# Kernel tuning notes

Measured on AMD Instinct MI355X. Metric: run time of the kernel, lower is better.

## Reference

```python
import jax, jax.numpy as jnp
import numpy as np

EMBED_DIM = 512
N_HEADS = 8
D_K = EMBED_DIM // N_HEADS

def _xavier(key, shape):
    fan_in, fan_out = shape[1], shape[0]
    limit = np.sqrt(6.0 / (fan_in + fan_out))
    return jax.random.uniform(key, shape, jnp.float32, -limit, limit)

def setup_inputs() -> dict:
    key = jax.random.key(0)
    ks = jax.random.split(key, 8)
    B, S, D = 2, 4096, EMBED_DIM
    return {
        "q": jax.random.normal(ks[0], (B, S, D), jnp.float32),
        "k": jax.random.normal(ks[1], (B, S, D), jnp.float32),
        "v": jax.random.normal(ks[2], (B, S, D), jnp.float32),
        "W_q": _xavier(ks[3], (D, D)),
        "W_k": _xavier(ks[4], (D, D)),
        "W_v": _xavier(ks[5], (D, D)),
        "W_o": _xavier(ks[6], (D, D)),
        "b_o": jnp.zeros((D,), jnp.float32),
    }

def reference(q, k, v, W_q, W_k, W_v, W_o, b_o):
    B, Sq, D = q.shape
    Sk = k.shape[1]
    # linear projections (torch Linear: x @ W.T)
    qh = (q @ W_q.T).reshape(B, Sq, N_HEADS, D_K).transpose(0, 2, 1, 3)
    kh = (k @ W_k.T).reshape(B, Sk, N_HEADS, D_K).transpose(0, 2, 1, 3)
    vh = (v @ W_v.T).reshape(B, Sk, N_HEADS, D_K).transpose(0, 2, 1, 3)
    scores = jnp.einsum('bhqd,bhkd->bhqk', qh, kh)  # [B,H,Sq,Sk]
    causal = jnp.triu(jnp.ones((Sq, Sk), bool), k=1)
    scores = jnp.where(causal, -jnp.inf, scores)
    attn = jax.nn.softmax(scores / np.sqrt(D_K), axis=-1)
    ctx = jnp.einsum('bhqk,bhkd->bhqd', attn, vh)
    ctx = ctx.transpose(0, 2, 1, 3).reshape(B, Sq, D)
    return ctx @ W_o.T + b_o
```

## Files before the change

### kernel.cpp

```cpp
#include <hip/hip_runtime.h>

typedef _Float16 f16;
typedef _Float16 f16x8 __attribute__((ext_vector_type(8)));
typedef _Float16 f16x4 __attribute__((ext_vector_type(4)));
typedef _Float16 f16x2 __attribute__((ext_vector_type(2)));
typedef float f32x4 __attribute__((ext_vector_type(4)));
typedef float f32x16 __attribute__((ext_vector_type(16)));
typedef unsigned int u32x2 __attribute__((ext_vector_type(2)));

#define S_TOK 4096
#define NB 2
#define NH 8
#define DKH 64
#define DMODEL 512

static __device__ __forceinline__ f32x4 mfma16(f16x8 a, f16x8 b, f32x4 c) {
    return __builtin_amdgcn_mfma_f32_16x16x32_f16(a, b, c, 0, 0, 0);
}
static __device__ __forceinline__ f32x16 mfma32(f16x8 a, f16x8 b, f32x16 c) {
    return __builtin_amdgcn_mfma_f32_32x32x16_f16(a, b, c, 0, 0, 0);
}
static __device__ __forceinline__ void gl16(const f16* g, f16* l) {
    __builtin_amdgcn_global_load_lds(
        (const __attribute__((address_space(1))) unsigned int*)g,
        (__attribute__((address_space(3))) unsigned int*)l, 16, 0, 0);
}

__global__ __launch_bounds__(256)
void proj_fused_kernel(const float* __restrict__ qx, const float* __restrict__ kx,
                       const float* __restrict__ vx,
                       const float* __restrict__ Wqp, const float* __restrict__ Wkp,
                       const float* __restrict__ Wvp,
                       f16* __restrict__ qo, f16* __restrict__ ko, f16* __restrict__ vo)
{
    const int mode = blockIdx.z;
    const float* x = (mode == 0) ? qx : (mode == 1) ? kx : vx;
    const float* W = (mode == 0) ? Wqp : (mode == 1) ? Wkp : Wvp;
    f16* out = (mode == 0) ? qo : (mode == 1) ? ko : vo;

    __shared__ f16 As[128 * 40];
    __shared__ f16 Bs[128 * 40];
    const int m0 = blockIdx.x * 128;
    const int n0 = blockIdx.y * 128;
    const int tid = threadIdx.x;
    const int wv = tid >> 6;
    const int lane = tid & 63;
    const int lr = lane & 15, lg = lane >> 4;
    const int wm = (wv >> 1) * 64, wn = (wv & 1) * 64;

    f32x4 acc[4][4];
#pragma unroll
    for (int i = 0; i < 4; ++i)
#pragma unroll
        for (int j = 0; j < 4; ++j) acc[i][j] = f32x4{0.f, 0.f, 0.f, 0.f};

    for (int kb = 0; kb < DMODEL; kb += 32) {
#pragma unroll
        for (int c = 0; c < 2; ++c) {
            const int chunk = tid + c * 256;
            const int row = chunk >> 2;
            const int col = (chunk & 3) * 8;
            const float* ga = x + (size_t)(m0 + row) * DMODEL + kb + col;
            float4 a0 = *(const float4*)ga;
            float4 a1 = *(const float4*)(ga + 4);
            f16x8 ha = { (f16)a0.x, (f16)a0.y, (f16)a0.z, (f16)a0.w,
                         (f16)a1.x, (f16)a1.y, (f16)a1.z, (f16)a1.w };
            *(f16x8*)(As + row * 40 + col) = ha;
            const float* gb = W + (size_t)(n0 + row) * DMODEL + kb + col;
            float4 b0 = *(const float4*)gb;
            float4 b1 = *(const float4*)(gb + 4);
            f16x8 hb = { (f16)b0.x, (f16)b0.y, (f16)b0.z, (f16)b0.w,
                         (f16)b1.x, (f16)b1.y, (f16)b1.z, (f16)b1.w };
            *(f16x8*)(Bs + row * 40 + col) = hb;
        }
        __syncthreads();
        f16x8 af[4], bf[4];
#pragma unroll
        for (int i = 0; i < 4; ++i)
            af[i] = *(const f16x8*)(As + (wm + 16 * i + lr) * 40 + 8 * lg);
#pragma unroll
        for (int j = 0; j < 4; ++j)
            bf[j] = *(const f16x8*)(Bs + (wn + 16 * j + lr) * 40 + 8 * lg);
#pragma unroll
        for (int i = 0; i < 4; ++i)
#pragma unroll
            for (int j = 0; j < 4; ++j)
                acc[i][j] = mfma16(af[i], bf[j], acc[i][j]);
        __syncthreads();
    }

#pragma unroll
    for (int i = 0; i < 4; ++i) {
        const int mbase = m0 + wm + 16 * i + 4 * lg;
#pragma unroll
        for (int j = 0; j < 4; ++j) {
            const int n = n0 + wn + 16 * j + lr;
            const int h = n >> 6, dk = n & 63;
            if (mode == 2) {
                const int b = mbase >> 12;
                const int s = mbase & 4095;
                f16x4 v4;
#pragma unroll
                for (int r = 0; r < 4; ++r) v4[r] = (f16)acc[i][j][r];
                *(f16x4*)(out + ((size_t)(b * NH + h) * DKH + dk) * S_TOK + s) = v4;
            } else {
                const float sc = (mode == 0) ? 0.1803368801111244f : 1.0f;
#pragma unroll
                for (int r = 0; r < 4; ++r) {
                    const int m = mbase + r;
                    const int b = m >> 12, s = m & 4095;
                    out[((size_t)(b * NH + h) * S_TOK + s) * DKH + dk] = (f16)(acc[i][j][r] * sc);
                }
            }
        }
    }
}

__global__ __launch_bounds__(256, 4)
void attn_kernel(const f16* __restrict__ qh, const f16* __restrict__ kh,
                 const f16* __restrict__ vt, f16* __restrict__ pO, float* __restrict__ pL)
{
    __shared__ f16 Ks[2][64 * 64];
    __shared__ f16 Vs[2][64 * 64];

    const int bid = blockIdx.x;
    const int bh = 2 * (bid & 7) + ((bid >> 3) & 1);
    const int j = (bid >> 4) & 31;
    const int cb = (bid >> 9) & 1;
    const int tid = threadIdx.x, wv = tid >> 6, lane = tid & 63;
    const int l31 = lane & 31, h = lane >> 5;
    const int swzl = (l31 & 7) ^ (((l31 >> 3) & 3) << 1);

    const f16* Qp = qh + (size_t)bh * S_TOK * DKH;
    const f16* Kp = kh + (size_t)bh * S_TOK * DKH;
    const f16* Vp = vt + (size_t)bh * DKH * S_TOK;

    const int srow = tid >> 3;
    const int sg = tid & 7;
    const int sgx = sg ^ ((srow & 7) ^ (((srow >> 3) & 3) << 1));

    int cur = 0;
    for (int seg = 0; seg < 2; ++seg) {
        const int qt = seg ? (31 - j) : j;
        const int cc = seg ? (3 - cb) : cb;
        const int T = 2 * qt + 2;
        const int tb = (cc * T) >> 2;
        const int te = ((cc + 1) * T) >> 2;
        const int qw = qt * 128 + 32 * wv + l31;
        const int unit = (bh * 32 + qt) * 4 + cc;

        f16x8 aq[4];
#pragma unroll
        for (int s = 0; s < 4; ++s)
            aq[s] = *(const f16x8*)(Qp + (size_t)qw * DKH + 16 * s + 8 * h);

        f32x16 accO0 = {}, accO1 = {};
        float mrow = -1e20f, lrow = 0.f;

        if (te > tb) {
            {
                const f16* kp1 = Kp + (size_t)(64 * tb + srow) * DKH + sgx * 8;
                gl16(kp1, &Ks[cur][wv * 512]);
                gl16(kp1 + 32 * DKH, &Ks[cur][2048 + wv * 512]);
                const f16* vp1 = Vp + (size_t)srow * S_TOK + 64 * tb + sgx * 8;
                gl16(vp1, &Vs[cur][wv * 512]);
                gl16(vp1 + (size_t)32 * S_TOK, &Vs[cur][2048 + wv * 512]);
            }
            for (int t = tb; t < te; ++t) {
                __syncthreads();
                if (t + 1 < te) {
                    const f16* kp1 = Kp + (size_t)(64 * (t + 1) + srow) * DKH + sgx * 8;
                    gl16(kp1, &Ks[cur ^ 1][wv * 512]);
                    gl16(kp1 + 32 * DKH, &Ks[cur ^ 1][2048 + wv * 512]);
                    const f16* vp1 = Vp + (size_t)srow * S_TOK + 64 * (t + 1) + sgx * 8;
                    gl16(vp1, &Vs[cur ^ 1][wv * 512]);
                    gl16(vp1 + (size_t)32 * S_TOK, &Vs[cur ^ 1][2048 + wv * 512]);
                }
                const f16* Kb = &Ks[cur][0];
                const f16* Vb = &Vs[cur][0];
                const bool diag = (t >= 2 * qt);

#pragma unroll
                for (int half = 0; half < 2; ++half) {
                    f32x16 accS = {};
                    __builtin_amdgcn_s_setprio(1);
#pragma unroll
                    for (int s = 0; s < 4; ++s) {
                        f16x8 ak = *(const f16x8*)(Kb + (32 * half + l31) * 64 +
                                                   ((2 * s + h) ^ swzl) * 8);
                        accS = mfma32(ak, aq[s], accS);
                    }
                    __builtin_amdgcn_s_setprio(0);

                    if (diag) {
#pragma unroll
                        for (int e = 0; e < 16; ++e) {
                            const int kvb = 64 * t + 32 * half + (e & 3) + 8 * (e >> 2) + 4 * h;
                            accS[e] = (kvb > qw) ? -1e30f : accS[e];
                        }
                    }

                    float m8a = fmaxf(fmaxf(accS[0], accS[1]), fmaxf(accS[2], accS[3]));
                    float m8b = fmaxf(fmaxf(accS[4], accS[5]), fmaxf(accS[6], accS[7]));
                    float m8c = fmaxf(fmaxf(accS[8], accS[9]), fmaxf(accS[10], accS[11]));
                    float m8d = fmaxf(fmaxf(accS[12], accS[13]), fmaxf(accS[14], accS[15]));
                    float tm = fmaxf(fmaxf(m8a, m8b), fmaxf(m8c, m8d));
                    tm = fmaxf(tm, __shfl_xor(tm, 32));
                    if (!__all(tm <= mrow + 8.f)) {
                        const float mn = fmaxf(mrow, tm);
                        const float sf = exp2f(mrow - mn);
                        lrow *= sf;
                        accO0 *= sf;  accO1 *= sf;
                        mrow = mn;
                    }

                    unsigned int Xd0[4], Xd1[4];
                    float ts4[4];
#pragma unroll
                    for (int g = 0; g < 4; ++g) {
                        float p0 = exp2f(accS[4 * g + 0] - mrow);
                        float p1 = exp2f(accS[4 * g + 1] - mrow);
                        float p2 = exp2f(accS[4 * g + 2] - mrow);
                        float p3 = exp2f(accS[4 * g + 3] - mrow);
                        ts4[g] = (p0 + p1) + (p2 + p3);
                        union { f16x2 hh; unsigned int u; } a0, a1;
                        a0.hh = f16x2{(f16)p0, (f16)p1};
                        a1.hh = f16x2{(f16)p2, (f16)p3};
                        Xd0[g] = a0.u;  Xd1[g] = a1.u;
                    }
                    float ts = (ts4[0] + ts4[1]) + (ts4[2] + ts4[3]);
                    ts += __shfl_xor(ts, 32);
                    lrow += ts;

                    __builtin_amdgcn_s_setprio(1);
#pragma unroll
                    for (int sp = 0; sp < 2; ++sp) {
                        const int spp = 2 * half + sp;
                        u32x2 rA = __builtin_amdgcn_permlane32_swap(Xd0[2 * sp], Xd0[2 * sp + 1], false, false);
                        u32x2 rB = __builtin_amdgcn_permlane32_swap(Xd1[2 * sp], Xd1[2 * sp + 1], false, false);
                        union { unsigned int u[4]; f16x8 v; } F;
                        F.u[0] = rA[0]; F.u[1] = rB[0]; F.u[2] = rA[1]; F.u[3] = rB[1];
                        f16x8 av0 = *(const f16x8*)(Vb + l31 * 64 + ((2 * spp + h) ^ swzl) * 8);
                        f16x8 av1 = *(const f16x8*)(Vb + (32 + l31) * 64 + ((2 * spp + h) ^ swzl) * 8);
                        accO0 = mfma32(av0, F.v, accO0);
                        accO1 = mfma32(av1, F.v, accO1);
                    }
                    __builtin_amdgcn_s_setprio(0);
                }
                cur ^= 1;
            }
        }

        const float invl = (lrow > 0.f) ? (1.f / lrow) : 0.f;
        f16* Ob = pO + ((size_t)unit * 128 + (32 * wv + l31)) * DKH;
#pragma unroll
        for (int g = 0; g < 4; ++g) {
            f16x4 o0, o1;
#pragma unroll
            for (int r = 0; r < 4; ++r) {
                o0[r] = (f16)(accO0[4 * g + r] * invl);
                o1[r] = (f16)(accO1[4 * g + r] * invl);
            }
            *(f16x4*)(Ob + 8 * g + 4 * h) = o0;
            *(f16x4*)(Ob + 32 + 8 * g + 4 * h) = o1;
        }
        if (h == 0)
            pL[unit * 128 + 32 * wv + l31] =
                (lrow > 0.f) ? (mrow + __log2f(lrow)) : -1e30f;
    }
}

__global__ __launch_bounds__(256)
void merge_kernel(const f16* __restrict__ pO, const float* __restrict__ pL,
                  f16* __restrict__ ctx)
{
    const int tid = threadIdx.x;
    const int R = blockIdx.x * 32 + (tid >> 3);
    const int dkg = tid & 7;
    const int bh = R >> 12, q = R & 4095;
    const int qt = q >> 7, qi = q & 127;
    const int ub = (bh * 32 + qt) * 4;

    float L[4];
#pragma unroll
    for (int c = 0; c < 4; ++c) L[c] = pL[(ub + c) * 128 + qi];
    float Lm = fmaxf(fmaxf(L[0], L[1]), fmaxf(L[2], L[3]));
    float w[4], wsum = 0.f;
#pragma unroll
    for (int c = 0; c < 4; ++c) { w[c] = exp2f(L[c] - Lm); wsum += w[c]; }
    const float inv = 1.f / wsum;

    float o[8];
#pragma unroll
    for (int i = 0; i < 8; ++i) o[i] = 0.f;
#pragma unroll
    for (int c = 0; c < 4; ++c) {
        f16x8 a = *(const f16x8*)(pO + ((size_t)(ub + c) * 128 + qi) * DKH + dkg * 8);
#pragma unroll
        for (int i = 0; i < 8; ++i) o[i] += w[c] * (float)a[i];
    }
    f16x8 ov;
#pragma unroll
    for (int i = 0; i < 8; ++i) ov[i] = (f16)(o[i] * inv);

    const int bb = bh >> 3, hh = bh & 7;
    *(f16x8*)(ctx + ((size_t)(bb * S_TOK + q)) * DMODEL + hh * DKH + dkg * 8) = ov;
}

__global__ __launch_bounds__(256)
void oproj_kernel(const f16* __restrict__ A, const float* __restrict__ W,
                  const float* __restrict__ bias, float* __restrict__ out)
{
    __shared__ f16 As[128 * 40];
    __shared__ f16 Bs[128 * 40];
    const int m0 = blockIdx.x * 128;
    const int n0 = blockIdx.y * 128;
    const int tid = threadIdx.x;
    const int wv = tid >> 6;
    const int lane = tid & 63;
    const int lr = lane & 15, lg = lane >> 4;
    const int wm = (wv >> 1) * 64, wn = (wv & 1) * 64;

    f32x4 acc[4][4];
#pragma unroll
    for (int i = 0; i < 4; ++i)
#pragma unroll
        for (int j = 0; j < 4; ++j) acc[i][j] = f32x4{0.f, 0.f, 0.f, 0.f};

    for (int kb = 0; kb < DMODEL; kb += 32) {
#pragma unroll
        for (int c = 0; c < 2; ++c) {
            const int chunk = tid + c * 256;
            const int row = chunk >> 2;
            const int col = (chunk & 3) * 8;
            *(f16x8*)(As + row * 40 + col) =
                *(const f16x8*)(A + (size_t)(m0 + row) * DMODEL + kb + col);
            const float* gb = W + (size_t)(n0 + row) * DMODEL + kb + col;
            float4 b0 = *(const float4*)gb;
            float4 b1 = *(const float4*)(gb + 4);
            f16x8 hb = { (f16)b0.x, (f16)b0.y, (f16)b0.z, (f16)b0.w,
                         (f16)b1.x, (f16)b1.y, (f16)b1.z, (f16)b1.w };
            *(f16x8*)(Bs + row * 40 + col) = hb;
        }
        __syncthreads();
        f16x8 af[4], bf[4];
#pragma unroll
        for (int i = 0; i < 4; ++i)
            af[i] = *(const f16x8*)(As + (wm + 16 * i + lr) * 40 + 8 * lg);
#pragma unroll
        for (int j = 0; j < 4; ++j)
            bf[j] = *(const f16x8*)(Bs + (wn + 16 * j + lr) * 40 + 8 * lg);
#pragma unroll
        for (int i = 0; i < 4; ++i)
#pragma unroll
            for (int j = 0; j < 4; ++j)
                acc[i][j] = mfma16(af[i], bf[j], acc[i][j]);
        __syncthreads();
    }

#pragma unroll
    for (int i = 0; i < 4; ++i) {
        const int mbase = m0 + wm + 16 * i + 4 * lg;
#pragma unroll
        for (int j = 0; j < 4; ++j) {
            const int n = n0 + wn + 16 * j + lr;
            const float bn = bias[n];
#pragma unroll
            for (int r = 0; r < 4; ++r) {
                const int m = mbase + r;
                out[(size_t)m * DMODEL + n] = acc[i][j][r] + bn;
            }
        }
    }
}

extern "C" void kernel_launch(void* const* d_in, const int* in_sizes, int n_in,
                              void* d_out, int out_size, void* d_ws, size_t ws_size,
                              hipStream_t stream) {
    const float* q  = (const float*)d_in[0];
    const float* k  = (const float*)d_in[1];
    const float* v  = (const float*)d_in[2];
    const float* Wq = (const float*)d_in[3];
    const float* Wk = (const float*)d_in[4];
    const float* Wv = (const float*)d_in[5];
    const float* Wo = (const float*)d_in[6];
    const float* bo = (const float*)d_in[7];
    float* out = (float*)d_out;

    const size_t per = (size_t)NB * NH * S_TOK * DKH;
    f16* qh  = (f16*)d_ws;
    f16* kh  = qh + per;
    f16* vt  = kh + per;
    f16* ctx = vt + per;
    f16* pO  = ctx + per;
    float* pL = (float*)(pO + (size_t)2048 * 128 * 64);

    proj_fused_kernel<<<dim3(64, 4, 3), 256, 0, stream>>>(q, k, v, Wq, Wk, Wv, qh, kh, vt);
    attn_kernel<<<dim3(1024), 256, 0, stream>>>(qh, kh, vt, pO, pL);
    merge_kernel<<<dim3(2048), 256, 0, stream>>>(pO, pL, ctx);
    oproj_kernel<<<dim3(64, 4), 256, 0, stream>>>(ctx, Wo, bo, out);
}
```

Measured before the change: 131.7 us.

## Load K/V fragments directly from global memory instead of LDS double-buffering

Removes the shared-memory double-buffered K/V staging (global_load_lds plus __syncthreads) from the attention kernel. Each wave now loads its K and V MFMA operands straight from global memory into registers, relying on L1/L2 caching for reuse across the four waves. Launch bounds drop from 4 to 3 blocks per SM to give more registers. This removes LDS traffic and block-wide barriers, but each wave now reads the same K/V tiles separately from global memory, with no explicit prefetch to hide load latency.

After: 187.4 us. 1.42x slower.

```diff
diff --git a/kernel.cpp b/kernel.cpp
--- a/kernel.cpp
+++ b/kernel.cpp
@@ -19,11 +19,6 @@
 }
 static __device__ __forceinline__ f32x16 mfma32(f16x8 a, f16x8 b, f32x16 c) {
     return __builtin_amdgcn_mfma_f32_32x32x16_f16(a, b, c, 0, 0, 0);
-}
-static __device__ __forceinline__ void gl16(const f16* g, f16* l) {
-    __builtin_amdgcn_global_load_lds(
-        (const __attribute__((address_space(1))) unsigned int*)g,
-        (__attribute__((address_space(3))) unsigned int*)l, 16, 0, 0);
 }
 
 __global__ __launch_bounds__(256)
@@ -116,30 +111,21 @@
     }
 }
 
-__global__ __launch_bounds__(256, 4)
+__global__ __launch_bounds__(256, 3)
 void attn_kernel(const f16* __restrict__ qh, const f16* __restrict__ kh,
                  const f16* __restrict__ vt, f16* __restrict__ pO, float* __restrict__ pL)
 {
-    __shared__ f16 Ks[2][64 * 64];
-    __shared__ f16 Vs[2][64 * 64];
-
     const int bid = blockIdx.x;
     const int bh = 2 * (bid & 7) + ((bid >> 3) & 1);
     const int j = (bid >> 4) & 31;
     const int cb = (bid >> 9) & 1;
     const int tid = threadIdx.x, wv = tid >> 6, lane = tid & 63;
     const int l31 = lane & 31, h = lane >> 5;
-    const int swzl = (l31 & 7) ^ (((l31 >> 3) & 3) << 1);
 
     const f16* Qp = qh + (size_t)bh * S_TOK * DKH;
     const f16* Kp = kh + (size_t)bh * S_TOK * DKH;
     const f16* Vp = vt + (size_t)bh * DKH * S_TOK;
 
-    const int srow = tid >> 3;
-    const int sg = tid & 7;
-    const int sgx = sg ^ ((srow & 7) ^ (((srow >> 3) & 3) << 1));
-
-    int cur = 0;
     for (int seg = 0; seg < 2; ++seg) {
         const int qt = seg ? (31 - j) : j;
         const int cc = seg ? (3 - cb) : cb;
@@ -157,98 +143,86 @@
         f32x16 accO0 = {}, accO1 = {};
         float mrow = -1e20f, lrow = 0.f;
 
-        if (te > tb) {
-            {
-                const f16* kp1 = Kp + (size_t)(64 * tb + srow) * DKH + sgx * 8;
-                gl16(kp1, &Ks[cur][wv * 512]);
-                gl16(kp1 + 32 * DKH, &Ks[cur][2048 + wv * 512]);
-                const f16* vp1 = Vp + (size_t)srow * S_TOK + 64 * tb + sgx * 8;
-                gl16(vp1, &Vs[cur][wv * 512]);
-                gl16(vp1 + (size_t)32 * S_TOK, &Vs[cur][2048 + wv * 512]);
+        const f16* Kl = Kp + (size_t)(64 * tb + l31) * DKH + 8 * h;
+        const f16* Vl0 = Vp + (size_t)l31 * S_TOK + 64 * tb + 8 * h;
+        const f16* Vl1 = Vp + (size_t)(32 + l31) * S_TOK + 64 * tb + 8 * h;
+
+        for (int t = tb; t < te; ++t) {
+            const bool diag = (t >= 2 * qt);
+#pragma unroll
+            for (int half = 0; half < 2; ++half) {
+                f16x8 ak0 = *(const f16x8*)(Kl + 32 * half * DKH);
+                f16x8 ak1 = *(const f16x8*)(Kl + 32 * half * DKH + 16);
+                f16x8 ak2 = *(const f16x8*)(Kl + 32 * half * DKH + 32);
+                f16x8 ak3 = *(const f16x8*)(Kl + 32 * half * DKH + 48);
+                f16x8 av00 = *(const f16x8*)(Vl0 + 32 * half);
+                f16x8 av01 = *(const f16x8*)(Vl0 + 32 * half + 16);
+                f16x8 av10 = *(const f16x8*)(Vl1 + 32 * half);
+                f16x8 av11 = *(const f16x8*)(Vl1 + 32 * half + 16);
+
+                f32x16 accS = {};
+                __builtin_amdgcn_s_setprio(1);
+                accS = mfma32(ak0, aq[0], accS);
+                accS = mfma32(ak1, aq[1], accS);
+                accS = mfma32(ak2, aq[2], accS);
+                accS = mfma32(ak3, aq[3], accS);
+                __builtin_amdgcn_s_setprio(0);
+
+                if (diag) {
+#pragma unroll
+                    for (int e = 0; e < 16; ++e) {
+                        const int kvb = 64 * t + 32 * half + (e & 3) + 8 * (e >> 2) + 4 * h;
+                        accS[e] = (kvb > qw) ? -1e30f : accS[e];
+                    }
+                }
+
+                float m8a = fmaxf(fmaxf(accS[0], accS[1]), fmaxf(accS[2], accS[3]));
+                float m8b = fmaxf(fmaxf(accS[4], accS[5]), fmaxf(accS[6], accS[7]));
+                float m8c = fmaxf(fmaxf(accS[8], accS[9]), fmaxf(accS[10], accS[11]));
+                float m8d = fmaxf(fmaxf(accS[12], accS[13]), fmaxf(accS[14], accS[15]));
+                float tm = fmaxf(fmaxf(m8a, m8b), fmaxf(m8c, m8d));
+                tm = fmaxf(tm, __shfl_xor(tm, 32));
+                if (!__all(tm <= mrow + 8.f)) {
+                    const float mn = fmaxf(mrow, tm);
+                    const float sf = exp2f(mrow - mn);
+                    lrow *= sf;
+                    accO0 *= sf;  accO1 *= sf;
+                    mrow = mn;
+                }
+
+                unsigned int Xd0[4], Xd1[4];
+                float ts4[4];
+#pragma unroll
+                for (int g = 0; g < 4; ++g) {
+                    float p0 = exp2f(accS[4 * g + 0] - mrow);
+                    float p1 = exp2f(accS[4 * g + 1] - mrow);
+                    float p2 = exp2f(accS[4 * g + 2] - mrow);
+                    float p3 = exp2f(accS[4 * g + 3] - mrow);
+                    ts4[g] = (p0 + p1) + (p2 + p3);
+                    union { f16x2 hh; unsigned int u; } a0, a1;
+                    a0.hh = f16x2{(f16)p0, (f16)p1};
+                    a1.hh = f16x2{(f16)p2, (f16)p3};
+                    Xd0[g] = a0.u;  Xd1[g] = a1.u;
+                }
+                float ts = (ts4[0] + ts4[1]) + (ts4[2] + ts4[3]);
+                ts += __shfl_xor(ts, 32);
+                lrow += ts;
+
+                __builtin_amdgcn_s_setprio(1);
+#pragma unroll
+                for (int sp = 0; sp < 2; ++sp) {
+                    u32x2 rA = __builtin_amdgcn_permlane32_swap(Xd0[2 * sp], Xd0[2 * sp + 1], false, false);
+                    u32x2 rB = __builtin_amdgcn_permlane32_swap(Xd1[2 * sp], Xd1[2 * sp + 1], false, false);
+                    union { unsigned int u[4]; f16x8 v; } F;
+                    F.u[0] = rA[0]; F.u[1] = rB[0]; F.u[2] = rA[1]; F.u[3] = rB[1];
+                    accO0 = mfma32(sp ? av01 : av00, F.v, accO0);
+                    accO1 = mfma32(sp ? av11 : av10, F.v, accO1);
+                }
+                __builtin_amdgcn_s_setprio(0);
             }
-            for (int t = tb; t < te; ++t) {
-                __syncthreads();
-                if (t + 1 < te) {
-                    const f16* kp1 = Kp + (size_t)(64 * (t + 1) + srow) * DKH + sgx * 8;
-                    gl16(kp1, &Ks[cur ^ 1][wv * 512]);
-                    gl16(kp1 + 32 * DKH, &Ks[cur ^ 1][2048 + wv * 512]);
-                    const f16* vp1 = Vp + (size_t)srow * S_TOK + 64 * (t + 1) + sgx * 8;
-                    gl16(vp1, &Vs[cur ^ 1][wv * 512]);
-                    gl16(vp1 + (size_t)32 * S_TOK, &Vs[cur ^ 1][2048 + wv * 512]);
-                }
-                const f16* Kb = &Ks[cur][0];
-                const f16* Vb = &Vs[cur][0];
-                const bool diag = (t >= 2 * qt);
-
-#pragma unroll
-                for (int half = 0; half < 2; ++half) {
-                    f32x16 accS = {};
-                    __builtin_amdgcn_s_setprio(1);
-#pragma unroll
-                    for (int s = 0; s < 4; ++s) {
-                        f16x8 ak = *(const f16x8*)(Kb + (32 * half + l31) * 64 +
-                                                   ((2 * s + h) ^ swzl) * 8);
-                        accS = mfma32(ak, aq[s], accS);
-                    }
-                    __builtin_amdgcn_s_setprio(0);
-
-                    if (diag) {
-#pragma unroll
-                        for (int e = 0; e < 16; ++e) {
-                            const int kvb = 64 * t + 32 * half + (e & 3) + 8 * (e >> 2) + 4 * h;
-                            accS[e] = (kvb > qw) ? -1e30f : accS[e];
-                        }
-                    }
-
-                    float m8a = fmaxf(fmaxf(accS[0], accS[1]), fmaxf(accS[2], accS[3]));
-                    float m8b = fmaxf(fmaxf(accS[4], accS[5]), fmaxf(accS[6], accS[7]));
-                    float m8c = fmaxf(fmaxf(accS[8], accS[9]), fmaxf(accS[10], accS[11]));
-                    float m8d = fmaxf(fmaxf(accS[12], accS[13]), fmaxf(accS[14], accS[15]));
-                    float tm = fmaxf(fmaxf(m8a, m8b), fmaxf(m8c, m8d));
-                    tm = fmaxf(tm, __shfl_xor(tm, 32));
-                    if (!__all(tm <= mrow + 8.f)) {
-                        const float mn = fmaxf(mrow, tm);
-                        const float sf = exp2f(mrow - mn);
-                        lrow *= sf;
-                        accO0 *= sf;  accO1 *= sf;
-                        mrow = mn;
-                    }
-
-                    unsigned int Xd0[4], Xd1[4];
-                    float ts4[4];
-#pragma unroll
-                    for (int g = 0; g < 4; ++g) {
-                        float p0 = exp2f(accS[4 * g + 0] - mrow);
-                        float p1 = exp2f(accS[4 * g + 1] - mrow);
-                        float p2 = exp2f(accS[4 * g + 2] - mrow);
-                        float p3 = exp2f(accS[4 * g + 3] - mrow);
-                        ts4[g] = (p0 + p1) + (p2 + p3);
-                        union { f16x2 hh; unsigned int u; } a0, a1;
-                        a0.hh = f16x2{(f16)p0, (f16)p1};
-                        a1.hh = f16x2{(f16)p2, (f16)p3};
-                        Xd0[g] = a0.u;  Xd1[g] = a1.u;
-                    }
-                    float ts = (ts4[0] + ts4[1]) + (ts4[2] + ts4[3]);
-                    ts += __shfl_xor(ts, 32);
-                    lrow += ts;
-
-                    __builtin_amdgcn_s_setprio(1);
-#pragma unroll
-                    for (int sp = 0; sp < 2; ++sp) {
-                        const int spp = 2 * half + sp;
-                        u32x2 rA = __builtin_amdgcn_permlane32_swap(Xd0[2 * sp], Xd0[2 * sp + 1], false, false);
-                        u32x2 rB = __builtin_amdgcn_permlane32_swap(Xd1[2 * sp], Xd1[2 * sp + 1], false, false);
-                        union { unsigned int u[4]; f16x8 v; } F;
-                        F.u[0] = rA[0]; F.u[1] = rB[0]; F.u[2] = rA[1]; F.u[3] = rB[1];
-                        f16x8 av0 = *(const f16x8*)(Vb + l31 * 64 + ((2 * spp + h) ^ swzl) * 8);
-                        f16x8 av1 = *(const f16x8*)(Vb + (32 + l31) * 64 + ((2 * spp + h) ^ swzl) * 8);
-                        accO0 = mfma32(av0, F.v, accO0);
-                        accO1 = mfma32(av1, F.v, accO1);
-                    }
-                    __builtin_amdgcn_s_setprio(0);
-                }
-                cur ^= 1;
-            }
+            Kl += 64 * DKH;
+            Vl0 += 64;
+            Vl1 += 64;
         }
 
         const float invl = (lrow > 0.f) ? (1.f / lrow) : 0.f;
```
